# Performance work log

Measured on AMD Instinct MI355X. Metric: run time of the kernel, lower is better.

The kernel has to match this reference:

```python
import jax, jax.numpy as jnp
import numpy as np

N_HEAD = 16

def setup_inputs() -> dict:
    key = jax.random.key(0)
    ks = jax.random.split(key, 5)
    B, T, C = 4, 1024, 1024
    d = C // N_HEAD
    x = jax.random.normal(ks[0], (B, T, C), dtype=jnp.float32)
    w_attn = jax.random.normal(ks[1], (C, 3 * C), dtype=jnp.float32) * 0.02
    w_proj = jax.random.normal(ks[2], (C, C), dtype=jnp.float32) * 0.02
    embk = 0.02 * jax.random.normal(ks[3], (T, d), dtype=jnp.float32)
    embv = 0.02 * jax.random.normal(ks[4], (T, d), dtype=jnp.float32)
    return {"x": x, "w_attn": w_attn, "w_proj": w_proj, "embk": embk, "embv": embv}

def reference(x, w_attn, w_proj, embk, embv):
    B, T, C = x.shape
    H = N_HEAD
    d = C // H
    qkv = x @ w_attn                                   # [B,T,3C]
    q, k, v = jnp.split(qkv, 3, axis=2)
    q = q.reshape(B, T, H, d).transpose(0, 2, 1, 3)     # [B,H,T,d]
    k = k.reshape(B, T, H, d).transpose(0, 2, 1, 3)
    v = v.reshape(B, T, H, d).transpose(0, 2, 1, 3)
    # relative positions, lower-triangular (0 above diagonal, masked anyway)
    idx = jnp.arange(T)
    rel = jnp.tril(idx[:, None] - idx[None, :])         # [T,T] int
    rk = embk[rel]                                      # [T,T,d]
    rv = embv[rel]                                      # [T,T,d]
    scale = 1.0 / np.sqrt(d).astype(np.float32)
    att = jnp.einsum('bhtd,bhsd->bhts', q, k) * scale \
        + jnp.einsum('bhtd,tsd->bhts', q, rk)           # [B,H,T,T]
    causal = (idx[None, :] <= idx[:, None])             # [T,T] bool
    att = jnp.where(causal[None, None], att, -jnp.inf)
    att = jax.nn.softmax(att, axis=-1)
    y = jnp.einsum('bhts,bhsd->bhtd', att, v) \
      + jnp.einsum('bhts,tsd->bhtd', att, rv)           # [B,H,T,d]
    y = y.transpose(0, 2, 1, 3).reshape(B, T, C)
    return y @ w_proj
```

## Files before the change

kernel.cpp:

```cpp
#include <hip/hip_runtime.h>
#include <math.h>

typedef unsigned short u16;
typedef short bf8 __attribute__((ext_vector_type(8)));
typedef float f32x4 __attribute__((ext_vector_type(4)));

__device__ __forceinline__ u16 f2b(float f) {
    union { float f; unsigned u; } x; x.f = f;
    return (u16)((x.u + 0x7FFFu + ((x.u >> 16) & 1u)) >> 16);
}
__device__ __forceinline__ float b2f(u16 b) {
    union { unsigned u; float f; } x; x.u = ((unsigned)b) << 16;
    return x.f;
}

__device__ __forceinline__ void async16(const void* g, void* l) {
    __builtin_amdgcn_global_load_lds(
        (const __attribute__((address_space(1))) unsigned int*)g,
        (__attribute__((address_space(3))) unsigned int*)l, 16, 0, 0);
}

__device__ __forceinline__ void cstore(float* p, float v) { *p = v; }
__device__ __forceinline__ void cstore(u16* p, float v) { *p = f2b(v); }

template<typename OutT>
__global__ __launch_bounds__(256) void gemm_mfma(const u16* __restrict__ A,
                                                 const u16* __restrict__ Bt,
                                                 OutT* __restrict__ C,
                                                 int M, int N, int K) {
    __shared__ __align__(16) u16 As[128 * 32];
    __shared__ __align__(16) u16 Bs[128 * 32];
    const int tid = threadIdx.x;
    const int w = tid >> 6, L = tid & 63;
    const int l15 = L & 15, quad = L >> 4;
    const int wm = (w >> 1) * 64, wn = (w & 1) * 64;
    const int row0 = blockIdx.y * 128, col0 = blockIdx.x * 128;
    const int laneRow = L >> 2, laneCol8 = (L & 3) * 8;

    f32x4 acc[4][4] = {};

    for (int k0 = 0; k0 < K; k0 += 32) {
        #pragma unroll
        for (int i = 0; i < 2; ++i) {
            const int seg = w * 2 + i;
            const int r = seg * 16 + laneRow;
            async16(&A[(size_t)(row0 + r) * K + k0 + laneCol8], &As[seg * 512 + L * 8]);
        }
        #pragma unroll
        for (int i = 0; i < 2; ++i) {
            const int seg = w * 2 + i;
            const int r = seg * 16 + laneRow;
            async16(&Bt[(size_t)(col0 + r) * K + k0 + laneCol8], &Bs[seg * 512 + L * 8]);
        }
        __syncthreads();
        bf8 a[4], b[4];
        #pragma unroll
        for (int mt = 0; mt < 4; ++mt)
            a[mt] = *(const bf8*)&As[(wm + mt * 16 + l15) * 32 + quad * 8];
        #pragma unroll
        for (int nt = 0; nt < 4; ++nt)
            b[nt] = *(const bf8*)&Bs[(wn + nt * 16 + l15) * 32 + quad * 8];
        #pragma unroll
        for (int mt = 0; mt < 4; ++mt)
            #pragma unroll
            for (int nt = 0; nt < 4; ++nt)
                acc[mt][nt] = __builtin_amdgcn_mfma_f32_16x16x32_bf16(
                    a[mt], b[nt], acc[mt][nt], 0, 0, 0);
        __syncthreads();
    }
    #pragma unroll
    for (int mt = 0; mt < 4; ++mt)
        #pragma unroll
        for (int nt = 0; nt < 4; ++nt) {
            const int col = col0 + wn + nt * 16 + l15;
            #pragma unroll
            for (int r = 0; r < 4; ++r) {
                const int row = row0 + wm + mt * 16 + quad * 4 + r;
                cstore(&C[(size_t)row * N + col], acc[mt][nt][r]);
            }
        }
}

template<typename OutT>
__global__ __launch_bounds__(256) void gemm_mfma64(const u16* __restrict__ A,
                                                   const u16* __restrict__ Bt,
                                                   OutT* __restrict__ C,
                                                   int M, int N, int K) {
    __shared__ __align__(16) u16 As[64 * 32];
    __shared__ __align__(16) u16 Bs[128 * 32];
    const int tid = threadIdx.x;
    const int w = tid >> 6, L = tid & 63;
    const int l15 = L & 15, quad = L >> 4;
    const int wm = (w >> 1) * 32, wn = (w & 1) * 64;
    const int row0 = blockIdx.y * 64, col0 = blockIdx.x * 128;
    const int laneRow = L >> 2, laneCol8 = (L & 3) * 8;

    f32x4 acc[2][4] = {};

    for (int k0 = 0; k0 < K; k0 += 32) {
        {
            const int r = w * 16 + laneRow;
            async16(&A[(size_t)(row0 + r) * K + k0 + laneCol8], &As[w * 512 + L * 8]);
        }
        #pragma unroll
        for (int i = 0; i < 2; ++i) {
            const int seg = w * 2 + i;
            const int r = seg * 16 + laneRow;
            async16(&Bt[(size_t)(col0 + r) * K + k0 + laneCol8], &Bs[seg * 512 + L * 8]);
        }
        __syncthreads();
        bf8 a[2], b[4];
        #pragma unroll
        for (int mt = 0; mt < 2; ++mt)
            a[mt] = *(const bf8*)&As[(wm + mt * 16 + l15) * 32 + quad * 8];
        #pragma unroll
        for (int nt = 0; nt < 4; ++nt)
            b[nt] = *(const bf8*)&Bs[(wn + nt * 16 + l15) * 32 + quad * 8];
        #pragma unroll
        for (int mt = 0; mt < 2; ++mt)
            #pragma unroll
            for (int nt = 0; nt < 4; ++nt)
                acc[mt][nt] = __builtin_amdgcn_mfma_f32_16x16x32_bf16(
                    a[mt], b[nt], acc[mt][nt], 0, 0, 0);
        __syncthreads();
    }
    #pragma unroll
    for (int mt = 0; mt < 2; ++mt)
        #pragma unroll
        for (int nt = 0; nt < 4; ++nt) {
            const int col = col0 + wn + nt * 16 + l15;
            #pragma unroll
            for (int r = 0; r < 4; ++r) {
                const int row = row0 + wm + mt * 16 + quad * 4 + r;
                cstore(&C[(size_t)row * N + col], acc[mt][nt][r]);
            }
        }
}

__global__ __launch_bounds__(256) void prep_all(const float* __restrict__ x,
                                                const float* __restrict__ embk,
                                                const float* __restrict__ embv,
                                                const float* __restrict__ w_attn,
                                                const float* __restrict__ w_proj,
                                                u16* __restrict__ xb,
                                                u16* __restrict__ EKP,
                                                u16* __restrict__ EVP,
                                                u16* __restrict__ waT,
                                                u16* __restrict__ wpT) {
    __shared__ u16 ts[64][65];
    const int bx = blockIdx.x;
    const int tid = threadIdx.x;
    if (bx < 4096) {
        int idx = bx * 256 + tid;
        const float4 v = ((const float4*)x)[idx];
        ((ushort4*)xb)[idx] = make_ushort4(f2b(v.x), f2b(v.y), f2b(v.z), f2b(v.w));
    } else if (bx < 4132) {
        int t = (bx - 4096) * 256 + tid;
        int L = t & 63, kc = (t >> 6) & 1, k16 = t >> 7;
        int l15 = L & 15, quad = L >> 4;
        int row = 1 + k16 * 16 + l15;
        int d = row - 128;
        int cl = d < 0 ? 0 : (d > 1023 ? 1023 : d);
        const float* p = embk + cl * 64 + kc * 32 + quad * 8;
        #pragma unroll
        for (int i = 0; i < 8; ++i) EKP[t * 8 + i] = f2b(p[i]);
    } else if (bx < 4168) {
        int t = (bx - 4132) * 256 + tid;
        int L = t & 63, rest = t >> 6;
        int c32 = rest % 36, tn = rest / 36;
        int l15 = L & 15, quad = L >> 4;
        #pragma unroll
        for (int i = 0; i < 8; ++i) {
            int c = c32 * 32 + quad * 8 + i;
            int d = c - 127;
            int cl = d < 0 ? 0 : (d > 1023 ? 1023 : d);
            EVP[t * 8 + i] = f2b(embv[cl * 64 + tn * 16 + l15]);
        }
    } else {
        const float* W; u16* WT; int Cc, t;
        if (bx < 4168 + 768) { t = bx - 4168; W = w_attn; WT = waT; Cc = 3072; }
        else                 { t = bx - 4936; W = w_proj; WT = wpT; Cc = 1024; }
        const int nx = Cc >> 6;
        const int c0 = (t % nx) * 64, r0 = (t / nx) * 64;
        for (int i = tid; i < 4096; i += 256) {
            int r = i >> 6, c = i & 63;
            ts[r][c] = f2b(W[(size_t)(r0 + r) * Cc + c0 + c]);
        }
        __syncthreads();
        for (int i = tid; i < 4096; i += 256) {
            int c = i >> 6, r = i & 63;
            WT[(size_t)(c0 + c) * 1024 + r0 + r] = ts[r][c];
        }
    }
}

__global__ __launch_bounds__(256) void pack_kv2(const u16* __restrict__ qkvb,
                                                u16* __restrict__ Kp,
                                                u16* __restrict__ Vp) {
    const int bx = blockIdx.x;
    if (bx < 2048) {
        int t = bx * 256 + threadIdx.x;
        int L = t & 63, kc = (t >> 6) & 1, s16 = (t >> 7) & 63, bh = t >> 13;
        int l15 = L & 15, quad = L >> 4;
        int b = bh >> 4, h = bh & 15;
        const u16* src = qkvb + (size_t)(b * 1024 + s16 * 16 + l15) * 3072
                       + 1024 + h * 64 + kc * 32 + quad * 8;
        u16* dst = Kp + (size_t)t * 8;
        #pragma unroll
        for (int i = 0; i < 8; ++i) dst[i] = f2b(b2f(src[i]) * 0.125f);
    } else {
        __shared__ __align__(16) u16 ts[64][40];
        const int tid = threadIdx.x;
        const int bxx = bx - 2048;
        const int bh = bxx >> 5, c32 = bxx & 31;
        const int b = bh >> 4, h = bh & 15;
        {
            const int sl = tid >> 3, d8 = (tid & 7) * 8;
            const u16* p = qkvb + (size_t)(b * 1024 + c32 * 32 + sl) * 3072
                         + 2048 + h * 64 + d8;
            uint4 v = *(const uint4*)p;
            const u16* e = (const u16*)&v;
            #pragma unroll
            for (int i = 0; i < 8; ++i) ts[d8 + i][sl] = e[i];
        }
        __syncthreads();
        const int tn = tid >> 6, L = tid & 63;
        const int l15 = L & 15, quad = L >> 4;
        const uint4 frag = *(const uint4*)&ts[tn * 16 + l15][quad * 8];
        *(uint4*)(Vp + ((size_t)(bh * 8192 + tn * 2048 + c32 * 64 + L)) * 8) = frag;
    }
}

__device__ const int d_S[17] = {0,1,2,4,6,9,12,16,20,25,30,36,42,49,56,64,72};
__device__ const int d_SB[16] = {0,0,0,0, 0,0,0,0, 2, 4, 6, 8,10,13,15,17};

__global__ __launch_bounds__(256) void attn_mfma(const u16* __restrict__ qkvb,
                                                 const u16* __restrict__ Kp,
                                                 const u16* __restrict__ Vp,
                                                 const u16* __restrict__ EKP,
                                                 const u16* __restrict__ EVP,
                                                 u16* __restrict__ yb,
                                                 float* __restrict__ po,
                                                 float* __restrict__ lsp) {
    __shared__ __align__(16) u16 slab_[4][2560];
    __shared__ __align__(16) u16 KVs[16384];

    const int tid = threadIdx.x;
    const int w = tid >> 6, L = tid & 63;
    const int l15 = L & 15, quad = L >> 4;
    const int blk = blockIdx.x;
    const int bh = blockIdx.y, b = bh >> 4, h = bh & 15;
    u16* S2l = slab_[w];
    u16* Pl  = slab_[w];
    u16* Ppl = slab_[w];

    const bf8* EKPF = (const bf8*)EKP;
    const bf8* EVPF = (const bf8*)EVP;

    bf8 qn[2];
    f32x4 o[4];
    float lsum[4];
    int t = -1, t0 = 0;

    auto flush = [&](int tt) {
        float lr[4];
        #pragma unroll
        for (int r = 0; r < 4; ++r) {
            float s = lsum[r];
            s += __shfl_xor(s, 1); s += __shfl_xor(s, 2);
            s += __shfl_xor(s, 4); s += __shfl_xor(s, 8);
            lr[r] = s;
        }
        const bool whole = (d_S[tt] >> 2) == ((d_S[tt + 1] - 1) >> 2);
        if (whole) {
            #pragma unroll
            for (int tn = 0; tn < 4; ++tn) {
                const int col = h * 64 + tn * 16 + l15;
                #pragma unroll
                for (int r = 0; r < 4; ++r) {
                    const int trow = tt * 64 + w * 16 + quad * 4 + r;
                    yb[(size_t)(b * 1024 + trow) * 1024 + col] = f2b(o[tn][r] / lr[r]);
                }
            }
        } else {
            const int slot = blk - (d_S[tt] >> 2);
            const size_t sidx = (size_t)(bh * 19 + d_SB[tt] + slot);
            float* pob = po + (sidx << 12);
            #pragma unroll
            for (int tn = 0; tn < 4; ++tn)
                #pragma unroll
                for (int r = 0; r < 4; ++r)
                    pob[(w * 16 + quad * 4 + r) * 64 + tn * 16 + l15] = o[tn][r];
            if (l15 == 0) {
                float* lsb = lsp + (sidx << 6);
                #pragma unroll
                for (int r = 0; r < 4; ++r) lsb[w * 16 + quad * 4 + r] = lr[r];
            }
        }
    };

    #pragma unroll 1
    for (int ui = 0; ui < 4; ++ui) {
        const int u = blk * 4 + ui;
        int nt = (t < 0) ? 0 : t;
        while (d_S[nt + 1] <= u) ++nt;
        if (nt != t) {
            if (t >= 0) flush(t);
            t = nt; t0 = t * 64;
            const int trow = t0 + w * 16 + l15;
            const u16* qp = qkvb + (size_t)(b * 1024 + trow) * 3072 + h * 64 + quad * 8;
            qn[0] = *(const bf8*)qp;
            qn[1] = *(const bf8*)(qp + 32);
            #pragma unroll
            for (int tn = 0; tn < 4; ++tn)
                #pragma unroll
                for (int j = 0; j < 4; ++j) o[tn][j] = 0.f;
            #pragma unroll
            for (int r = 0; r < 4; ++r) lsum[r] = 0.f;
        }
        const int c = u - d_S[t];
        const int s0 = c << 7;
        const int diff = t0 - s0;

        __syncthreads();

        {
            const size_t kbase = ((size_t)(bh * 64 + (s0 >> 4)) << 1) * 512;
            #pragma unroll
            for (int i = 0; i < 4; ++i)
                async16(Kp + kbase + (i * 256 + tid) * 8, &KVs[(i * 256 + tid) * 8]);
        }

        f32x4 s2[9] = {};
        {
            const int kb = (diff >> 4) + w;
            #pragma unroll
            for (int j = 0; j < 9; ++j) {
                #pragma unroll
                for (int kc = 0; kc < 2; ++kc)
                    s2[j] = __builtin_amdgcn_mfma_f32_16x16x32_bf16(
                        qn[kc], EKPF[(((kb + j) << 1) + kc) * 64 + L], s2[j], 0, 0, 0);
            }
        }
        #pragma unroll
        for (int j = 0; j < 9; ++j)
            #pragma unroll
            for (int r = 0; r < 4; ++r)
                S2l[(quad * 4 + r) * 148 + j * 16 + l15] = f2b(s2[j][r]);

        __builtin_amdgcn_sched_barrier(0);
        {
            const int vb = bh * 128 + (s0 >> 5);
            #pragma unroll
            for (int i = 0; i < 4; ++i)
                async16(Vp + ((size_t)(vb + i * 32) * 512 + tid * 8),
                        &KVs[8192 + i * 2048 + tid * 8]);
        }

        asm volatile("s_waitcnt vmcnt(4)" ::: "memory");
        __builtin_amdgcn_s_barrier();
        __builtin_amdgcn_sched_barrier(0);

        f32x4 s1[8];
        __builtin_amdgcn_s_setprio(1);
        #pragma unroll
        for (int tn = 0; tn < 8; ++tn) {
            f32x4 z = {};
            #pragma unroll
            for (int kc = 0; kc < 2; ++kc) {
                const bf8 kf = *(const bf8*)&KVs[((tn << 1) + kc) * 512 + L * 8];
                z = __builtin_amdgcn_mfma_f32_16x16x32_bf16(qn[kc], kf, z, 0, 0, 0);
            }
            s1[tn] = z;
        }
        __builtin_amdgcn_s_setprio(0);

        #pragma unroll
        for (int tn = 0; tn < 8; ++tn) {
            const int cl = tn * 16 + l15;
            #pragma unroll
            for (int r = 0; r < 4; ++r) {
                const int row = quad * 4 + r;
                float v = s1[tn][r] + b2f(S2l[row * 148 + (row - cl + 127)]);
                if (cl > diff + w * 16 + row) v = -1e30f;
                float p = __expf(v - 4.0f);
                s1[tn][r] = p;
                lsum[r] += p;
            }
        }

        #pragma unroll
        for (int tn = 0; tn < 8; ++tn) {
            const int cl = tn * 16 + l15;
            #pragma unroll
            for (int r = 0; r < 4; ++r) {
                const int row = quad * 4 + r;
                Pl[((cl >> 5) << 9) + (((cl >> 3) & 3) << 7) + (row << 3) + (cl & 7)]
                    = f2b(s1[tn][r]);
            }
        }
        bf8 pa[4];
        #pragma unroll
        for (int kc = 0; kc < 4; ++kc) pa[kc] = ((const bf8*)Pl)[kc * 64 + L];

        #pragma unroll
        for (int i = 0; i < 5; ++i)
            ((uint4*)Ppl)[i * 64 + L] = make_uint4(0, 0, 0, 0);
        #pragma unroll
        for (int tn = 0; tn < 8; ++tn) {
            const int cl = tn * 16 + l15;
            #pragma unroll
            for (int r = 0; r < 4; ++r) {
                const int row = quad * 4 + r;
                const int dc = (w & 1) * 16 + row - cl + 127;
                Ppl[((dc >> 5) << 9) + (((dc >> 3) & 3) << 7) + (row << 3) + (dc & 7)]
                    = f2b(s1[tn][r]);
            }
        }

        __syncthreads();
        __builtin_amdgcn_sched_barrier(0);

        __builtin_amdgcn_s_setprio(1);
        {
            #pragma unroll
            for (int tn = 0; tn < 4; ++tn) {
                #pragma unroll
                for (int kc = 0; kc < 4; ++kc) {
                    const bf8 vf = *(const bf8*)&KVs[8192 + (tn * 4 + kc) * 512 + L * 8];
                    o[tn] = __builtin_amdgcn_mfma_f32_16x16x32_bf16(
                        pa[kc], vf, o[tn], 0, 0, 0);
                }
            }
        }
        {
            bf8 pb[5];
            #pragma unroll
            for (int kc = 0; kc < 5; ++kc) pb[kc] = ((const bf8*)Ppl)[kc * 64 + L];
            const int eb = (diff >> 5) + (w >> 1);
            #pragma unroll
            for (int tn = 0; tn < 4; ++tn) {
                #pragma unroll
                for (int kc = 0; kc < 5; ++kc)
                    o[tn] = __builtin_amdgcn_mfma_f32_16x16x32_bf16(
                        pb[kc], EVPF[(tn * 36 + eb + kc) * 64 + L], o[tn], 0, 0, 0);
            }
        }
        __builtin_amdgcn_s_setprio(0);
    }
    flush(t);
}

__global__ __launch_bounds__(256) void attn_reduce(const float* __restrict__ po,
                                                   const float* __restrict__ lsp,
                                                   u16* __restrict__ yb) {
    const int gi = blockIdx.x;
    const int t = (gi == 0) ? 4 : (gi + 7);
    const int bh = blockIdx.y, b = bh >> 4, h = bh & 15;
    const int ns = (t == 12) ? 3 : 2;
    const size_t base = (size_t)(bh * 19 + d_SB[t]);
    const float* pob = po + (base << 12);
    const float* lsb = lsp + (base << 6);
    #pragma unroll 1
    for (int i = 0; i < 16; ++i) {
        const int idx = i * 256 + threadIdx.x;
        const int row = idx >> 6, col = idx & 63;
        float acc = 0.f, lacc = 0.f;
        for (int s = 0; s < ns; ++s) {
            acc  += pob[(s << 12) + idx];
            lacc += lsb[(s << 6) + row];
        }
        yb[(size_t)(b * 1024 + t * 64 + row) * 1024 + h * 64 + col] = f2b(acc / lacc);
    }
}

extern "C" void kernel_launch(void* const* d_in, const int* in_sizes, int n_in,
                              void* d_out, int out_size, void* d_ws, size_t ws_size,
                              hipStream_t stream) {
    const float* x      = (const float*)d_in[0];
    const float* w_attn = (const float*)d_in[1];
    const float* w_proj = (const float*)d_in[2];
    const float* embk   = (const float*)d_in[3];
    const float* embv   = (const float*)d_in[4];
    float* out = (float*)d_out;

    u16* wsb   = (u16*)d_ws;
    u16* qkvb  = wsb;
    u16* xb    = qkvb + 12582912;
    u16* ymidb = xb;
    u16* waT   = xb + 4194304;
    u16* wpT   = waT + 3145728;
    u16* Vt    = wpT + 1048576;
    u16* Kp    = Vt + 4194304;
    u16* Vp    = Kp + 4194304;
    u16* EKP   = Vp + 4194304;
    u16* EVP   = EKP + 73728;
    float* po  = (float*)(EVP + 73728);
    float* lsp = po + 4980736;

    prep_all<<<dim3(5192), 256, 0, stream>>>(x, embk, embv, w_attn, w_proj,
                                             xb, EKP, EVP, waT, wpT);
    gemm_mfma<u16><<<dim3(24, 32), 256, 0, stream>>>(xb, waT, qkvb, 4096, 3072, 1024);
    pack_kv2<<<dim3(4096), 256, 0, stream>>>(qkvb, Kp, Vp);
    attn_mfma<<<dim3(18, 64), 256, 0, stream>>>(qkvb, Kp, Vp, EKP, EVP, ymidb, po, lsp);
    attn_reduce<<<dim3(9, 64), 256, 0, stream>>>(po, lsp, ymidb);
    gemm_mfma64<float><<<dim3(8, 64), 256, 0, stream>>>(ymidb, wpT, out, 4096, 1024, 1024);
}
```

Baseline: 239.1 us.

## Prefetch next K tile during PV phase and specialize unmasked softmax path

Moves the async K tile load for the next work unit to just after the P/V barrier, so it overlaps with the PV MFMAs and the next iteration's relative-position score computation. Barriers now wait on vmcnt(0) at both points. The constant -4 softmax offset is folded into the MFMA accumulator's initial value. Fully unmasked tiles (diff>=128) take a branch without the causal compare. The risks are the extra waits at the barriers and possible reuse hazards on the K buffer region.

```diff
diff --git a/kernel.cpp b/kernel.cpp
--- a/kernel.cpp
+++ b/kernel.cpp
@@ -299,6 +299,17 @@
         }
     };
 
+    {
+        const int u0 = blk * 4;
+        int tt = 0;
+        while (d_S[tt + 1] <= u0) ++tt;
+        const int s00 = (u0 - d_S[tt]) << 7;
+        const size_t kbase = ((size_t)(bh * 64 + (s00 >> 4)) << 1) * 512;
+        #pragma unroll
+        for (int i = 0; i < 4; ++i)
+            async16(Kp + kbase + (i * 256 + tid) * 8, &KVs[(i * 256 + tid) * 8]);
+    }
+
     #pragma unroll 1
     for (int ui = 0; ui < 4; ++ui) {
         const int u = blk * 4 + ui;
@@ -322,15 +333,6 @@
         const int s0 = c << 7;
         const int diff = t0 - s0;
 
-        __syncthreads();
-
-        {
-            const size_t kbase = ((size_t)(bh * 64 + (s0 >> 4)) << 1) * 512;
-            #pragma unroll
-            for (int i = 0; i < 4; ++i)
-                async16(Kp + kbase + (i * 256 + tid) * 8, &KVs[(i * 256 + tid) * 8]);
-        }
-
         f32x4 s2[9] = {};
         {
             const int kb = (diff >> 4) + w;
@@ -348,7 +350,10 @@
             for (int r = 0; r < 4; ++r)
                 S2l[(quad * 4 + r) * 148 + j * 16 + l15] = f2b(s2[j][r]);
 
+        asm volatile("s_waitcnt vmcnt(0)" ::: "memory");
+        __builtin_amdgcn_s_barrier();
         __builtin_amdgcn_sched_barrier(0);
+
         {
             const int vb = bh * 128 + (s0 >> 5);
             #pragma unroll
@@ -357,15 +362,11 @@
                         &KVs[8192 + i * 2048 + tid * 8]);
         }
 
-        asm volatile("s_waitcnt vmcnt(4)" ::: "memory");
-        __builtin_amdgcn_s_barrier();
-        __builtin_amdgcn_sched_barrier(0);
-
         f32x4 s1[8];
         __builtin_amdgcn_s_setprio(1);
         #pragma unroll
         for (int tn = 0; tn < 8; ++tn) {
-            f32x4 z = {};
+            f32x4 z = {-4.f, -4.f, -4.f, -4.f};
             #pragma unroll
             for (int kc = 0; kc < 2; ++kc) {
                 const bf8 kf = *(const bf8*)&KVs[((tn << 1) + kc) * 512 + L * 8];
@@ -375,17 +376,32 @@
         }
         __builtin_amdgcn_s_setprio(0);
 
-        #pragma unroll
-        for (int tn = 0; tn < 8; ++tn) {
-            const int cl = tn * 16 + l15;
-            #pragma unroll
-            for (int r = 0; r < 4; ++r) {
-                const int row = quad * 4 + r;
-                float v = s1[tn][r] + b2f(S2l[row * 148 + (row - cl + 127)]);
-                if (cl > diff + w * 16 + row) v = -1e30f;
-                float p = __expf(v - 4.0f);
-                s1[tn][r] = p;
-                lsum[r] += p;
+        if (diff < 128) {
+            #pragma unroll
+            for (int tn = 0; tn < 8; ++tn) {
+                const int cl = tn * 16 + l15;
+                #pragma unroll
+                for (int r = 0; r < 4; ++r) {
+                    const int row = quad * 4 + r;
+                    float v = s1[tn][r] + b2f(S2l[row * 148 + (row - cl + 127)]);
+                    if (cl > diff + w * 16 + row) v = -1e30f;
+                    const float p = __expf(v);
+                    s1[tn][r] = p;
+                    lsum[r] += p;
+                }
+            }
+        } else {
+            #pragma unroll
+            for (int tn = 0; tn < 8; ++tn) {
+                const int cl = tn * 16 + l15;
+                #pragma unroll
+                for (int r = 0; r < 4; ++r) {
+                    const int row = quad * 4 + r;
+                    const float v = s1[tn][r] + b2f(S2l[row * 148 + (row - cl + 127)]);
+                    const float p = __expf(v);
+                    s1[tn][r] = p;
+                    lsum[r] += p;
+                }
             }
         }
 
@@ -418,8 +434,20 @@
             }
         }
 
-        __syncthreads();
+        asm volatile("s_waitcnt vmcnt(0)" ::: "memory");
+        __builtin_amdgcn_s_barrier();
         __builtin_amdgcn_sched_barrier(0);
+
+        if (ui < 3) {
+            const int un = u + 1;
+            int tn2 = t;
+            while (d_S[tn2 + 1] <= un) ++tn2;
+            const int s0n = (un - d_S[tn2]) << 7;
+            const size_t kbase = ((size_t)(bh * 64 + (s0n >> 4)) << 1) * 512;
+            #pragma unroll
+            for (int i = 0; i < 4; ++i)
+                async16(Kp + kbase + (i * 256 + tid) * 8, &KVs[(i * 256 + tid) * 8]);
+        }
 
         __builtin_amdgcn_s_setprio(1);
         {
```

Measured after the change: 296.0 us. 1.24x slower.
